# Kernel tuning notes

Measured on AMD Instinct MI355X. Metric: run time of the kernel, lower is better.

## Reference

```python
import jax, jax.numpy as jnp
import numpy as np

B, S, D = 16, 2048, 256

def setup_inputs() -> dict:
    key = jax.random.key(0)
    ks = jax.random.split(key, 7)
    scale = 1.0 / np.sqrt(D)
    return {
        "x": jax.random.normal(ks[0], (B, S, D), dtype=jnp.float32),
        "Wq": jax.random.normal(ks[1], (D, D), dtype=jnp.float32) * scale,
        "bq": jax.random.normal(ks[2], (D,), dtype=jnp.float32) * 0.01,
        "Wk": jax.random.normal(ks[3], (D, D), dtype=jnp.float32) * scale,
        "bk": jax.random.normal(ks[4], (D,), dtype=jnp.float32) * 0.01,
        "Wv": jax.random.normal(ks[5], (D, D), dtype=jnp.float32) * scale,
        "bv": jax.random.normal(ks[6], (D,), dtype=jnp.float32) * 0.01,
    }

def reference(x, Wq, bq, Wk, bk, Wv, bv):
    # q,k,v: [B,S,D]
    q = x @ Wq + bq
    k = x @ Wk + bk
    v = x @ Wv + bv
    inv_sqrt_d = jnp.asarray(1.0 / np.sqrt(x.shape[-1]), dtype=x.dtype)
    energy = jnp.einsum('bqd,bkd->bqk', q, k) * inv_sqrt_d  # [B,S,S]
    attn = jax.nn.softmax(energy, axis=-1)
    weighted = jnp.einsum('bqk,bkd->bqd', attn, v)  # [B,S,D]
    return weighted.sum(axis=1)  # [B,D]
```

## Files before the change

### kernel.cpp

```cpp
#include <hip/hip_runtime.h>
#include <hip/hip_bf16.h>

typedef __bf16 bf16_t;
typedef bf16_t bf16x8 __attribute__((ext_vector_type(8)));
typedef float  f32x4  __attribute__((ext_vector_type(4)));

constexpr int S = 2048, D = 256;


__device__ __forceinline__ float fast_exp2(float x) {
    return __builtin_amdgcn_exp2f(x);
}

__global__ void wt_kernel(const float* __restrict__ Wq, const float* __restrict__ Wk,
                          bf16_t* __restrict__ wtf) {
    int idx = blockIdx.x * 256 + threadIdx.x;
    int w    = idx >> 13;
    int rem  = idx & 8191;
    int nt   = rem >> 9;
    int rem2 = rem & 511;
    int ks   = rem2 >> 6;
    int lane = rem2 & 63;
    int lm = lane & 15, lg = lane >> 4;
    const float* Wsrc = (w == 0) ? Wq : Wk;
    int col = nt * 16 + lm, krow = ks * 32 + lg * 8;
    bf16x8 o;
#pragma unroll
    for (int j = 0; j < 8; j++) o[j] = (bf16_t)Wsrc[(krow + j) * 256 + col];
    *(bf16x8*)(wtf + (size_t)idx * 8) = o;
}

__global__ __launch_bounds__(256) void proj_kernel(
    const float* __restrict__ x, const bf16_t* __restrict__ wtf,
    const float* __restrict__ bq, const float* __restrict__ bk,
    bf16_t* __restrict__ qo, bf16_t* __restrict__ ko) {
    __shared__ bf16_t sb_all[4][4480];
    int w    = blockIdx.y;
    int tid  = threadIdx.x;
    int wave = tid >> 6, lane = tid & 63, lm = lane & 15, lg = lane >> 4;
    int m0   = blockIdx.x * 128;
    const bf16_t* wb   = wtf + w * 65536;
    const float*  bias = (w == 0) ? bq : bk;

    f32x4 acc[2][16];
#pragma unroll
    for (int s = 0; s < 2; s++)
#pragma unroll
        for (int nt = 0; nt < 16; nt++) acc[s][nt] = f32x4{0.f, 0.f, 0.f, 0.f};

    const float* xr0 = x + (size_t)(m0 + wave * 32 + lm) * 256 + lg * 8;
    const float* xr1 = xr0 + 16 * 256;

    for (int ks = 0; ks < 8; ks++) {
        bf16x8 af[2];
        {
            float4 a0 = *(const float4*)(xr0 + ks * 32);
            float4 a1 = *(const float4*)(xr0 + ks * 32 + 4);
            float4 b0 = *(const float4*)(xr1 + ks * 32);
            float4 b1 = *(const float4*)(xr1 + ks * 32 + 4);
            af[0][0] = (bf16_t)a0.x; af[0][1] = (bf16_t)a0.y;
            af[0][2] = (bf16_t)a0.z; af[0][3] = (bf16_t)a0.w;
            af[0][4] = (bf16_t)a1.x; af[0][5] = (bf16_t)a1.y;
            af[0][6] = (bf16_t)a1.z; af[0][7] = (bf16_t)a1.w;
            af[1][0] = (bf16_t)b0.x; af[1][1] = (bf16_t)b0.y;
            af[1][2] = (bf16_t)b0.z; af[1][3] = (bf16_t)b0.w;
            af[1][4] = (bf16_t)b1.x; af[1][5] = (bf16_t)b1.y;
            af[1][6] = (bf16_t)b1.z; af[1][7] = (bf16_t)b1.w;
        }
#pragma unroll
        for (int nt = 0; nt < 16; nt++) {
            bf16x8 bfr = *(const bf16x8*)(wb + (size_t)(nt * 8 + ks) * 512 + lane * 8);
            acc[0][nt] = __builtin_amdgcn_mfma_f32_16x16x32_bf16(af[0], bfr, acc[0][nt], 0, 0, 0);
            acc[1][nt] = __builtin_amdgcn_mfma_f32_16x16x32_bf16(af[1], bfr, acc[1][nt], 0, 0, 0);
        }
    }

    bf16_t* sb = sb_all[wave];
    int bglob = m0 >> 11;
    bf16_t* dst = (w == 0) ? qo : ko;
#pragma unroll
    for (int s = 0; s < 2; s++) {
#pragma unroll
        for (int nt = 0; nt < 16; nt++) {
            int col = nt * 16 + lm;
            float bval = bias[col];
#pragma unroll
            for (int r = 0; r < 4; r++)
                sb[(lg * 4 + r) * 280 + col] = (bf16_t)(acc[s][nt][r] + bval);
        }
        int qb = ((m0 & 2047) >> 4) + wave * 2 + s;
#pragma unroll
        for (int ks = 0; ks < 8; ks++) {
            bf16x8 v8 = *(const bf16x8*)&sb[lm * 280 + ks * 32 + lg * 8];
            *(bf16x8*)(dst + ((size_t)((bglob * 128 + qb) * 8 + ks)) * 512 + lane * 8) = v8;
        }
    }
}

template <int PASS>
__global__ __launch_bounds__(512) void attn_pass(
    const bf16_t* __restrict__ q, const bf16_t* __restrict__ kmat,
    float* __restrict__ lpart, float* __restrict__ wpart) {
    __shared__ bf16_t kst[2][16384];
    __shared__ bf16_t wacc[8][512];

    int tid  = threadIdx.x;
    int wave = tid >> 6, lane = tid & 63, lm = lane & 15, lg = lane >> 4;
    int i  = blockIdx.x;
    int b  = ((i & 7) << 1) | ((i >> 8) & 1);
    int qt = (i >> 3) & 7;
    int kh = (i >> 6) & 3;

    bf16x8 af[2][8];
#pragma unroll
    for (int s = 0; s < 2; s++) {
        const bf16_t* qb = q + ((size_t)((b * 128 + qt * 16 + wave * 2 + s) * 8)) * 512;
#pragma unroll
        for (int ks = 0; ks < 8; ks++)
            af[s][ks] = *(const bf16x8*)(qb + ks * 512 + lane * 8);
    }

    float rinv[2][4];
    if (PASS == 2) {
#pragma unroll
        for (int s = 0; s < 2; s++)
#pragma unroll
            for (int r = 0; r < 4; r++) {
                int row = qt * 256 + wave * 32 + s * 16 + lg * 4 + r;
                float l = 0.f;
#pragma unroll
                for (int k2 = 0; k2 < 4; k2++)
                    l += lpart[(size_t)(k2 * 16 + b) * 2048 + row];
                rinv[s][r] = 1.0f / l;
            }
    }

    float lsum[2][4];
#pragma unroll
    for (int s = 0; s < 2; s++)
#pragma unroll
        for (int r = 0; r < 4; r++) lsum[s][r] = 0.f;

    constexpr float SCL = 0.0625f * 1.44269504f;
    const bf16_t* kb_base = kmat + (size_t)(b * 128 + kh * 32) * 4096;

    bf16x8 stg[4];
#pragma unroll
    for (int u = 0; u < 4; u++)
        stg[u] = *(const bf16x8*)(kb_base + (size_t)(u * 512 + tid) * 8);

    for (int t = 0; t < 8; t++) {
        int p = t & 1;
#pragma unroll
        for (int u = 0; u < 4; u++)
            *(bf16x8*)&kst[p][(u * 512 + tid) * 8] = stg[u];
        if (t < 7) {
#pragma unroll
            for (int u = 0; u < 4; u++)
                stg[u] = *(const bf16x8*)(kb_base + (size_t)(t + 1) * 16384 + (u * 512 + tid) * 8);
        }
        __syncthreads();

        f32x4 sacc[2][4];
#pragma unroll
        for (int s = 0; s < 2; s++)
#pragma unroll
            for (int kb = 0; kb < 4; kb++) sacc[s][kb] = f32x4{0.f, 0.f, 0.f, 0.f};
#pragma unroll
        for (int ks = 0; ks < 8; ks++) {
#pragma unroll
            for (int kb = 0; kb < 4; kb++) {
                bf16x8 bfr = *(const bf16x8*)&kst[p][(kb * 8 + ks) * 512 + lane * 8];
                sacc[0][kb] = __builtin_amdgcn_mfma_f32_16x16x32_bf16(af[0][ks], bfr, sacc[0][kb], 0, 0, 0);
                sacc[1][kb] = __builtin_amdgcn_mfma_f32_16x16x32_bf16(af[1][ks], bfr, sacc[1][kb], 0, 0, 0);
            }
        }

        if (PASS == 1) {
#pragma unroll
            for (int s = 0; s < 2; s++)
#pragma unroll
                for (int kb = 0; kb < 4; kb++)
#pragma unroll
                    for (int r = 0; r < 4; r++)
                        lsum[s][r] += fast_exp2(sacc[s][kb][r] * SCL);
        } else {
            float wv[4] = {0.f, 0.f, 0.f, 0.f};
#pragma unroll
            for (int s = 0; s < 2; s++)
#pragma unroll
                for (int kb = 0; kb < 4; kb++)
#pragma unroll
                    for (int r = 0; r < 4; r++)
                        wv[kb] += fast_exp2(sacc[s][kb][r] * SCL) * rinv[s][r];
#pragma unroll
            for (int kb = 0; kb < 4; kb++) {
                float vsum = wv[kb];
                vsum += __shfl_xor(vsum, 16);
                vsum += __shfl_xor(vsum, 32);
                if (lg == 0) wacc[wave][t * 64 + kb * 16 + lm] = (bf16_t)vsum;
            }
        }
    }

    if (PASS == 1) {
#pragma unroll
        for (int s = 0; s < 2; s++)
#pragma unroll
            for (int r = 0; r < 4; r++) {
                float v2 = lsum[s][r];
                v2 += __shfl_xor(v2, 1);
                v2 += __shfl_xor(v2, 2);
                v2 += __shfl_xor(v2, 4);
                v2 += __shfl_xor(v2, 8);
                if (lm == 0) {
                    int row = qt * 256 + wave * 32 + s * 16 + lg * 4 + r;
                    lpart[(size_t)(kh * 16 + b) * 2048 + row] = v2;
                }
            }
    } else {
        __syncthreads();
        float sum = 0.f;
#pragma unroll
        for (int w2 = 0; w2 < 8; w2++) sum += (float)wacc[w2][tid];
        wpart[(size_t)(qt * 16 + b) * 2048 + kh * 512 + tid] = sum;
    }
}

__global__ __launch_bounds__(256) void xsum_kernel(
    const float* __restrict__ wpart, const float* __restrict__ x,
    float* __restrict__ gpart) {
    __shared__ float ldsw[128];
    int b = blockIdx.x >> 4, kseg = blockIdx.x & 15, tid = threadIdx.x;
    if (tid < 128) {
        int key = kseg * 128 + tid;
        float s = 0.f;
#pragma unroll
        for (int qt = 0; qt < 8; qt++) s += wpart[(size_t)(qt * 16 + b) * 2048 + key];
        ldsw[tid] = s;
    }
    __syncthreads();
    const float* xb = x + ((size_t)b * 2048 + kseg * 128) * 256;
    float acc = 0.f;
#pragma unroll 8
    for (int t = 0; t < 128; t++) acc += ldsw[t] * xb[(size_t)t * 256 + tid];
    gpart[(size_t)(kseg * 16 + b) * 256 + tid] = acc;
}

__global__ __launch_bounds__(256) void final_kernel(
    const float* __restrict__ gpart, const float* __restrict__ Wv,
    const float* __restrict__ bv, float* __restrict__ out) {
    __shared__ float yl[256];
    int b = blockIdx.x, tid = threadIdx.x;
    float s = 0.f;
#pragma unroll
    for (int ks = 0; ks < 16; ks++) s += gpart[(size_t)(ks * 16 + b) * 256 + tid];
    yl[tid] = s;
    __syncthreads();
    float acc = 0.f;
#pragma unroll 4
    for (int c = 0; c < 256; c++) acc += yl[c] * Wv[c * 256 + tid];
    out[b * 256 + tid] = acc + 2048.0f * bv[tid];
}

extern "C" void kernel_launch(void* const* d_in, const int* in_sizes, int n_in,
                              void* d_out, int out_size, void* d_ws, size_t ws_size,
                              hipStream_t stream) {
    const float* x  = (const float*)d_in[0];
    const float* Wq = (const float*)d_in[1];
    const float* bq = (const float*)d_in[2];
    const float* Wk = (const float*)d_in[3];
    const float* bk = (const float*)d_in[4];
    const float* Wv = (const float*)d_in[5];
    const float* bv = (const float*)d_in[6];
    float* out = (float*)d_out;

    char* ws = (char*)d_ws;
    bf16_t* wtf   = (bf16_t*)(ws);
    bf16_t* q     = (bf16_t*)(ws + 262144);
    bf16_t* kmat  = (bf16_t*)(ws + 17039360);
    float*  lpart = (float*) (ws + 33816576);
    float*  wpart = (float*) (ws + 34340864);
    float*  gpart = (float*) (ws + 35389440);

    wt_kernel<<<dim3(64), dim3(256), 0, stream>>>(Wq, Wk, wtf);
    proj_kernel<<<dim3(256, 2), dim3(256), 0, stream>>>(x, wtf, bq, bk, q, kmat);
    attn_pass<1><<<dim3(512), dim3(512), 0, stream>>>(q, kmat, lpart, wpart);
    attn_pass<2><<<dim3(512), dim3(512), 0, stream>>>(q, kmat, lpart, wpart);
    xsum_kernel<<<dim3(256), dim3(256), 0, stream>>>(wpart, x, gpart);
    final_kernel<<<dim3(16), dim3(256), 0, stream>>>(gpart, Wv, bv, out);
}
```

Measured before the change: 199.6 us.

## Double query rows per attention block to halve K-tile loads

Each attention block now handles 512 query rows (4 strips per wave) instead of 256, so every staged K tile in LDS is reused across twice as many queries. The grid shrinks from 512 to 256 blocks, wpart shrinks to 4 query tiles, and xsum reads fewer partials. The score computation is split into two halves per K tile to bound accumulator registers, and launch_bounds asks for 2 blocks per CU. The risks are higher register pressure from 32 A-fragment registers and fewer blocks to fill the 256 CUs.

```diff
diff --git a/kernel.cpp b/kernel.cpp
--- a/kernel.cpp
+++ b/kernel.cpp
@@ -98,7 +98,7 @@
 }
 
 template <int PASS>
-__global__ __launch_bounds__(512) void attn_pass(
+__global__ __launch_bounds__(512, 2) void attn_pass(
     const bf16_t* __restrict__ q, const bf16_t* __restrict__ kmat,
     float* __restrict__ lpart, float* __restrict__ wpart) {
     __shared__ bf16_t kst[2][16384];
@@ -106,27 +106,28 @@
 
     int tid  = threadIdx.x;
     int wave = tid >> 6, lane = tid & 63, lm = lane & 15, lg = lane >> 4;
-    int i  = blockIdx.x;
-    int b  = ((i & 7) << 1) | ((i >> 8) & 1);
-    int qt = (i >> 3) & 7;
-    int kh = (i >> 6) & 3;
-
-    bf16x8 af[2][8];
-#pragma unroll
-    for (int s = 0; s < 2; s++) {
-        const bf16_t* qb = q + ((size_t)((b * 128 + qt * 16 + wave * 2 + s) * 8)) * 512;
+    int i    = blockIdx.x;
+    int idx2 = i >> 3;
+    int qt   = idx2 & 3;
+    int kh   = (idx2 >> 2) & 3;
+    int b    = (i & 7) * 2 + (idx2 >> 4);
+
+    bf16x8 af[4][8];
+#pragma unroll
+    for (int s = 0; s < 4; s++) {
+        const bf16_t* qb = q + ((size_t)((b * 128 + qt * 32 + wave * 4 + s) * 8)) * 512;
 #pragma unroll
         for (int ks = 0; ks < 8; ks++)
             af[s][ks] = *(const bf16x8*)(qb + ks * 512 + lane * 8);
     }
 
-    float rinv[2][4];
+    float rinv[4][4];
     if (PASS == 2) {
 #pragma unroll
-        for (int s = 0; s < 2; s++)
+        for (int s = 0; s < 4; s++)
 #pragma unroll
             for (int r = 0; r < 4; r++) {
-                int row = qt * 256 + wave * 32 + s * 16 + lg * 4 + r;
+                int row = qt * 512 + wave * 64 + s * 16 + lg * 4 + r;
                 float l = 0.f;
 #pragma unroll
                 for (int k2 = 0; k2 < 4; k2++)
@@ -135,9 +136,9 @@
             }
     }
 
-    float lsum[2][4];
-#pragma unroll
-    for (int s = 0; s < 2; s++)
+    float lsum[4][4];
+#pragma unroll
+    for (int s = 0; s < 4; s++)
 #pragma unroll
         for (int r = 0; r < 4; r++) lsum[s][r] = 0.f;
 
@@ -161,51 +162,52 @@
         }
         __syncthreads();
 
-        f32x4 sacc[2][4];
-#pragma unroll
-        for (int s = 0; s < 2; s++)
-#pragma unroll
-            for (int kb = 0; kb < 4; kb++) sacc[s][kb] = f32x4{0.f, 0.f, 0.f, 0.f};
-#pragma unroll
-        for (int ks = 0; ks < 8; ks++) {
-#pragma unroll
-            for (int kb = 0; kb < 4; kb++) {
-                bf16x8 bfr = *(const bf16x8*)&kst[p][(kb * 8 + ks) * 512 + lane * 8];
-                sacc[0][kb] = __builtin_amdgcn_mfma_f32_16x16x32_bf16(af[0][ks], bfr, sacc[0][kb], 0, 0, 0);
-                sacc[1][kb] = __builtin_amdgcn_mfma_f32_16x16x32_bf16(af[1][ks], bfr, sacc[1][kb], 0, 0, 0);
-            }
-        }
-
-        if (PASS == 1) {
-#pragma unroll
-            for (int s = 0; s < 2; s++)
-#pragma unroll
-                for (int kb = 0; kb < 4; kb++)
-#pragma unroll
-                    for (int r = 0; r < 4; r++)
-                        lsum[s][r] += fast_exp2(sacc[s][kb][r] * SCL);
-        } else {
-            float wv[4] = {0.f, 0.f, 0.f, 0.f};
-#pragma unroll
-            for (int s = 0; s < 2; s++)
-#pragma unroll
-                for (int kb = 0; kb < 4; kb++)
-#pragma unroll
-                    for (int r = 0; r < 4; r++)
-                        wv[kb] += fast_exp2(sacc[s][kb][r] * SCL) * rinv[s][r];
-#pragma unroll
-            for (int kb = 0; kb < 4; kb++) {
-                float vsum = wv[kb];
-                vsum += __shfl_xor(vsum, 16);
-                vsum += __shfl_xor(vsum, 32);
-                if (lg == 0) wacc[wave][t * 64 + kb * 16 + lm] = (bf16_t)vsum;
+#pragma unroll
+        for (int h = 0; h < 2; h++) {
+            f32x4 sacc[4][2];
+#pragma unroll
+            for (int s = 0; s < 4; s++) {
+                sacc[s][0] = f32x4{0.f, 0.f, 0.f, 0.f};
+                sacc[s][1] = f32x4{0.f, 0.f, 0.f, 0.f};
+            }
+#pragma unroll
+            for (int ks = 0; ks < 8; ks++) {
+                bf16x8 b0 = *(const bf16x8*)&kst[p][((h * 2 + 0) * 8 + ks) * 512 + lane * 8];
+                bf16x8 b1 = *(const bf16x8*)&kst[p][((h * 2 + 1) * 8 + ks) * 512 + lane * 8];
+#pragma unroll
+                for (int s = 0; s < 4; s++) {
+                    sacc[s][0] = __builtin_amdgcn_mfma_f32_16x16x32_bf16(af[s][ks], b0, sacc[s][0], 0, 0, 0);
+                    sacc[s][1] = __builtin_amdgcn_mfma_f32_16x16x32_bf16(af[s][ks], b1, sacc[s][1], 0, 0, 0);
+                }
+            }
+            if (PASS == 1) {
+#pragma unroll
+                for (int s = 0; s < 4; s++)
+#pragma unroll
+                    for (int j = 0; j < 2; j++)
+#pragma unroll
+                        for (int r = 0; r < 4; r++)
+                            lsum[s][r] += fast_exp2(sacc[s][j][r] * SCL);
+            } else {
+#pragma unroll
+                for (int j = 0; j < 2; j++) {
+                    float wv = 0.f;
+#pragma unroll
+                    for (int s = 0; s < 4; s++)
+#pragma unroll
+                        for (int r = 0; r < 4; r++)
+                            wv += fast_exp2(sacc[s][j][r] * SCL) * rinv[s][r];
+                    wv += __shfl_xor(wv, 16);
+                    wv += __shfl_xor(wv, 32);
+                    if (lg == 0) wacc[wave][t * 64 + (h * 2 + j) * 16 + lm] = (bf16_t)wv;
+                }
             }
         }
     }
 
     if (PASS == 1) {
 #pragma unroll
-        for (int s = 0; s < 2; s++)
+        for (int s = 0; s < 4; s++)
 #pragma unroll
             for (int r = 0; r < 4; r++) {
                 float v2 = lsum[s][r];
@@ -214,7 +216,7 @@
                 v2 += __shfl_xor(v2, 4);
                 v2 += __shfl_xor(v2, 8);
                 if (lm == 0) {
-                    int row = qt * 256 + wave * 32 + s * 16 + lg * 4 + r;
+                    int row = qt * 512 + wave * 64 + s * 16 + lg * 4 + r;
                     lpart[(size_t)(kh * 16 + b) * 2048 + row] = v2;
                 }
             }
@@ -236,7 +238,7 @@
         int key = kseg * 128 + tid;
         float s = 0.f;
 #pragma unroll
-        for (int qt = 0; qt < 8; qt++) s += wpart[(size_t)(qt * 16 + b) * 2048 + key];
+        for (int qt = 0; qt < 4; qt++) s += wpart[(size_t)(qt * 16 + b) * 2048 + key];
         ldsw[tid] = s;
     }
     __syncthreads();
@@ -281,12 +283,12 @@
     bf16_t* kmat  = (bf16_t*)(ws + 17039360);
     float*  lpart = (float*) (ws + 33816576);
     float*  wpart = (float*) (ws + 34340864);
-    float*  gpart = (float*) (ws + 35389440);
+    float*  gpart = (float*) (ws + 34865152);
 
     wt_kernel<<<dim3(64), dim3(256), 0, stream>>>(Wq, Wk, wtf);
     proj_kernel<<<dim3(256, 2), dim3(256), 0, stream>>>(x, wtf, bq, bk, q, kmat);
-    attn_pass<1><<<dim3(512), dim3(512), 0, stream>>>(q, kmat, lpart, wpart);
-    attn_pass<2><<<dim3(512), dim3(512), 0, stream>>>(q, kmat, lpart, wpart);
+    attn_pass<1><<<dim3(256), dim3(512), 0, stream>>>(q, kmat, lpart, wpart);
+    attn_pass<2><<<dim3(256), dim3(512), 0, stream>>>(q, kmat, lpart, wpart);
     xsum_kernel<<<dim3(256), dim3(256), 0, stream>>>(wpart, x, gpart);
     final_kernel<<<dim3(16), dim3(256), 0, stream>>>(gpart, Wv, bv, out);
 }
```

After: 191.3 us. -4.2%, faster.
